# Performance work log

Hardware: AMD Instinct MI355X
Metric: run time of the kernel (lower is better)

## Reference

```python
import jax, jax.numpy as jnp
import numpy as np

HID, E, S, L_CAP, EPS = 768, 1536, 128, 512, 1e-5


def _rope_seq(x):
    """RoPE along axis 1. x: [b, n, 2, s]."""
    n, s = x.shape[1], x.shape[-1]
    half = s // 2
    inv_freq = jnp.power(10000.0, -jnp.arange(half, dtype=x.dtype) / half)  # [half]
    sinusoid = jnp.arange(n, dtype=x.dtype)[:, None, None] * inv_freq       # [n,1,half]
    sin, cos = jnp.sin(sinusoid), jnp.cos(sinusoid)
    x1, x2 = jnp.split(x, 2, axis=-1)
    return jnp.concatenate([x1 * cos - x2 * sin, x2 * cos + x1 * sin], axis=-1)


def setup_inputs() -> dict:
    key = jax.random.key(0)
    ks = jax.random.split(key, 6)
    B, L = 32, 512
    return {
        "x": jax.random.normal(ks[0], (B, L, HID), dtype=jnp.float32),
        "ln_gamma": jnp.ones((HID,), jnp.float32),
        "ln_beta": jnp.zeros((HID,), jnp.float32),
        "uv_W": jax.random.normal(ks[1], (HID, 2 * E + S), jnp.float32) * 0.02,
        "uv_b": jnp.zeros((2 * E + S,), jnp.float32),
        "gamma_qk": jax.random.normal(ks[2], (2, S), jnp.float32) * 0.02,
        "beta_qk": jnp.zeros((2, S), jnp.float32),
        "w_rel": jax.random.normal(ks[3], (2 * L_CAP - 1,), jnp.float32) * 0.02,
        "o_W": jax.random.normal(ks[4], (E, HID), jnp.float32) * 0.02,
        "o_b": jnp.zeros((HID,), jnp.float32),
    }


def reference(x, ln_gamma, ln_beta, uv_W, uv_b, gamma_qk, beta_qk, w_rel, o_W, o_b):
    L = x.shape[1]
    shortcut = x
    # LayerNorm
    mu = jnp.mean(x, axis=-1, keepdims=True)
    var = jnp.mean(jnp.square(x - mu), axis=-1, keepdims=True)
    xn = (x - mu) * jax.lax.rsqrt(var + EPS) * ln_gamma + ln_beta
    # uv projection + silu, split into u, v, base
    uv = jax.nn.silu(xn @ uv_W + uv_b)                       # [b, n, 2e+s]
    u, v, base = jnp.split(uv, [E, 2 * E], axis=-1)          # [b,n,e], [b,n,e], [b,n,s]
    # per-head affine then RoPE -> q, k
    base = base[..., None, :] * gamma_qk + beta_qk           # [b, n, 2, s]
    base = _rope_seq(base)
    q, k = base[..., 0, :], base[..., 1, :]
    # relu^2 attention kernel with Toeplitz relative position bias
    qk = jnp.einsum('bnd,bmd->bnm', q, k)
    idx = jnp.arange(L)
    bias = w_rel[idx[None, :] - idx[:, None] + L - 1]        # bias[i,j] = w[j-i+L-1]
    kernel = jnp.square(jax.nn.relu(qk / L + bias))
    # gated value aggregation + output projection + residual
    out = u * jnp.einsum('bnm,bme->bne', kernel, v)
    out = out @ o_W + o_b
    return out + shortcut
```

## Files before the change

kernel.cpp:

```cpp
#include <hip/hip_runtime.h>
#include <hip/hip_bf16.h>
#include <math.h>

typedef __bf16 bf16x8 __attribute__((ext_vector_type(8)));
typedef float f32x4 __attribute__((ext_vector_type(4)));
typedef unsigned short u16x4 __attribute__((ext_vector_type(4)));

#define AS1P const __attribute__((address_space(1))) void*
#define AS3P __attribute__((address_space(3))) void*

__device__ __forceinline__ float b2f(unsigned short h) {
    unsigned int u = ((unsigned int)h) << 16;
    return __builtin_bit_cast(float, u);
}
__device__ __forceinline__ unsigned short f2b(float f) {
    unsigned int u = __builtin_bit_cast(unsigned int, f);
    u += 0x7FFFu + ((u >> 16) & 1u);
    return (unsigned short)(u >> 16);
}
__device__ __forceinline__ float silu(float c) {
    return c * __builtin_amdgcn_rcpf(1.0f + __expf(-c));
}

__global__ __launch_bounds__(256) void k_convT(const float* __restrict__ src,
                                               unsigned short* __restrict__ dst,
                                               int R, int C) {
    __shared__ float tile[32][33];
    int tx = threadIdx.x, ty = threadIdx.y;
    int r0 = blockIdx.y << 5, c0 = blockIdx.x << 5;
#pragma unroll
    for (int i = 0; i < 4; ++i)
        tile[ty + 8 * i][tx] = src[(long long)(r0 + ty + 8 * i) * C + c0 + tx];
    __syncthreads();
#pragma unroll
    for (int i = 0; i < 4; ++i)
        dst[(long long)(c0 + ty + 8 * i) * R + r0 + tx] = f2b(tile[tx][ty + 8 * i]);
}

__global__ __launch_bounds__(256) void k_ln(const float* __restrict__ x,
                                            const float* __restrict__ g,
                                            const float* __restrict__ b,
                                            unsigned short* __restrict__ xn) {
    int row = blockIdx.x;
    int t = threadIdx.x;
    const float* xr = x + (long long)row * 768;
    float v0 = xr[t], v1 = xr[t + 256], v2 = xr[t + 512];
    float s = v0 + v1 + v2;
    float q = v0 * v0 + v1 * v1 + v2 * v2;
#pragma unroll
    for (int off = 32; off > 0; off >>= 1) {
        s += __shfl_xor(s, off);
        q += __shfl_xor(q, off);
    }
    __shared__ float ss[4], sq[4];
    int w = t >> 6;
    if ((t & 63) == 0) { ss[w] = s; sq[w] = q; }
    __syncthreads();
    float S_ = ss[0] + ss[1] + ss[2] + ss[3];
    float Q_ = sq[0] + sq[1] + sq[2] + sq[3];
    float mu = S_ * (1.0f / 768.0f);
    float var = Q_ * (1.0f / 768.0f) - mu * mu;
    float rs = rsqrtf(var + 1e-5f);
    unsigned short* xo = xn + (long long)row * 768;
    xo[t]       = f2b((v0 - mu) * rs * g[t]       + b[t]);
    xo[t + 256] = f2b((v1 - mu) * rs * g[t + 256] + b[t + 256]);
    xo[t + 512] = f2b((v2 - mu) * rs * g[t + 512] + b[t + 512]);
}

__global__ __launch_bounds__(128) void k_rope(const unsigned short* __restrict__ bS,
                                              const float* __restrict__ gqk,
                                              const float* __restrict__ bqk,
                                              unsigned short* __restrict__ q,
                                              unsigned short* __restrict__ k) {
    int row = blockIdx.x;
    int l = row & 511;
    int s = threadIdx.x;
    int j = s & 63;
    int partner = s ^ 64;
    float b0 = b2f(bS[(long long)row * 128 + s]);
    float bp = b2f(bS[(long long)row * 128 + partner]);
    float invf = __expf((float)j * -0.14391156831f);
    float th = (float)l * invf;
    float sn, cs;
    __sincosf(th, &sn, &cs);
    float sign = (s < 64) ? -1.0f : 1.0f;
    float preq  = b0 * gqk[s]           + bqk[s];
    float preqp = bp * gqk[partner]     + bqk[partner];
    q[(long long)row * 128 + s] = f2b(preq * cs + sign * preqp * sn);
    float prek  = b0 * gqk[128 + s]       + bqk[128 + s];
    float prekp = bp * gqk[128 + partner] + bqk[128 + partner];
    k[(long long)row * 128 + s] = f2b(prek * cs + sign * prekp * sn);
}

__global__ __launch_bounds__(256) void k_qk(const unsigned short* __restrict__ A,
                                            const unsigned short* __restrict__ B,
                                            const float* __restrict__ wrel,
                                            unsigned short* __restrict__ P) {
    __shared__ __align__(16) unsigned short As[128 * 64];
    __shared__ __align__(16) unsigned short Bs[128 * 64];
    int t = threadIdx.x;
    int w = t >> 6, lane = t & 63;
    int wr = w >> 1, wc = w & 1;
    int bx = blockIdx.x, by = blockIdx.y, bz = blockIdx.z;
    const unsigned short* Ab = A + (long long)bz * 512 * 128 + (long long)by * 128 * 128;
    const unsigned short* Bb = B + (long long)bz * 512 * 128 + (long long)bx * 128 * 128;

    f32x4 acc[4][4];
#pragma unroll
    for (int m = 0; m < 4; ++m)
#pragma unroll
        for (int n = 0; n < 4; ++n) acc[m][n] = (f32x4){0.f, 0.f, 0.f, 0.f};

    int rowA = (w << 3) + (lane >> 3);
    int colA = (lane & 7) << 3;

    for (int k0 = 0; k0 < 128; k0 += 64) {
#pragma unroll
        for (int i = 0; i < 4; ++i) {
            int r = (i << 5) + rowA;
            __builtin_amdgcn_global_load_lds(
                (AS1P)(Ab + (long long)r * 128 + k0 + colA),
                (AS3P)(&As[(i << 11) + (w << 9)]), 16, 0, 0);
            __builtin_amdgcn_global_load_lds(
                (AS1P)(Bb + (long long)r * 128 + k0 + colA),
                (AS3P)(&Bs[(i << 11) + (w << 9)]), 16, 0, 0);
        }
        __syncthreads();
#pragma unroll
        for (int ks = 0; ks < 2; ++ks) {
            bf16x8 af[4], bfr[4];
#pragma unroll
            for (int m = 0; m < 4; ++m)
                af[m] = *(const bf16x8*)&As[((wr << 6) + (m << 4) + (lane & 15)) * 64 +
                                            (ks << 5) + ((lane >> 4) << 3)];
#pragma unroll
            for (int n = 0; n < 4; ++n)
                bfr[n] = *(const bf16x8*)&Bs[((wc << 6) + (n << 4) + (lane & 15)) * 64 +
                                             (ks << 5) + ((lane >> 4) << 3)];
#pragma unroll
            for (int m = 0; m < 4; ++m)
#pragma unroll
                for (int n = 0; n < 4; ++n)
                    acc[m][n] = __builtin_amdgcn_mfma_f32_16x16x32_bf16(bfr[n], af[m],
                                                                        acc[m][n], 0, 0, 0);
        }
        __syncthreads();
    }

    int c15 = lane & 15, qq = lane >> 4;
    int rowb = (by << 7) + (wr << 6) + c15;
    int colb = (bx << 7) + (wc << 6) + (qq << 2);
#pragma unroll
    for (int m = 0; m < 4; ++m) {
#pragma unroll
        for (int n = 0; n < 4; ++n) {
            int grow = rowb + (m << 4);
            int gcol = colb + (n << 4);
            f32x4 a = acc[m][n];
            int base = gcol - grow + 511;
            u16x4 o;
#pragma unroll
            for (int i = 0; i < 4; ++i) {
                float val = a[i] * (1.0f / 512.0f) + wrel[base + i];
                val = fmaxf(val, 0.0f);
                o[i] = f2b(val * val);
            }
            *(u16x4*)(P + ((long long)(bz * 512 + grow)) * 512 + gcol) = o;
        }
    }
}

__device__ __forceinline__ bf16x8 ldsb(const char* p) {
    bf16x8 r;
    unsigned int off =
        (unsigned int)(unsigned long long)(__attribute__((address_space(3))) const void*)p;
    asm volatile("ds_read_b128 %0, %1" : "=v"(r) : "v"(off));
    return r;
}
__device__ __forceinline__ void stage64(const unsigned short* __restrict__ g, int ldk,
                                        char* lds, int r0, int w, int lane) {
    int row = r0 + (w << 3) + (lane >> 3);
    int colb = (lane & 7) << 4;
    int scolb = colb ^ ((row & 7) << 4);
    __builtin_amdgcn_global_load_lds(
        (AS1P)((const char*)g + (long long)row * (ldk * 2) + scolb),
        (AS3P)(lds + (r0 << 7) + (w << 10)), 16, 0, 0);
}

template <bool SWAP, int NT>
__device__ __forceinline__ void kloopP(const unsigned short* __restrict__ Ab,
                                       const unsigned short* __restrict__ Bb,
                                       char* A0, char* A1, char* B0, char* B1,
                                       f32x4 (&acc)[8][4], int tid, int wr, int wc,
                                       int o0, int o1) {
    constexpr int K = NT * 64;
    int w = tid >> 6, lane = tid & 63;
    const int abase = wr * 16384;
    const int bbase = wc * 8192;
    bf16x8 afA[2], afB[2], bfrA[4], bfrB[4];

#define STAGE(gA, gB, bufA, bufB)                          \
    stage64(gA, K, bufA, 0, w, lane);                      \
    stage64(gA, K, bufA, 64, w, lane);                     \
    stage64(gA, K, bufA, 128, w, lane);                    \
    stage64(gA, K, bufA, 192, w, lane);                    \
    stage64(gB, K, bufB, 0, w, lane);                      \
    stage64(gB, K, bufB, 64, w, lane);                     \
    stage64(gB, K, bufB, 128, w, lane);                    \
    stage64(gB, K, bufB, 192, w, lane);
#define LA(DST, mp, OKS, BUF)                              \
    DST[0] = ldsb((BUF) + abase + (mp) * 4096 + (OKS));    \
    DST[1] = ldsb((BUF) + abase + (mp) * 4096 + 2048 + (OKS));
#define LB(DST, OKS, BUF)                                  \
    DST[0] = ldsb((BUF) + bbase + (OKS));                  \
    DST[1] = ldsb((BUF) + bbase + 2048 + (OKS));           \
    DST[2] = ldsb((BUF) + bbase + 4096 + (OKS));           \
    DST[3] = ldsb((BUF) + bbase + 6144 + (OKS));
#define WAITL(N)                                           \
    asm volatile("s_waitcnt lgkmcnt(" #N ")" ::: "memory");\
    __builtin_amdgcn_sched_barrier(0);
#define MM(mp, BFR, AF)                                                               \
    __builtin_amdgcn_s_setprio(1);                                                    \
    _Pragma("unroll") for (int j_ = 0; j_ < 2; ++j_)                                  \
        _Pragma("unroll") for (int n_ = 0; n_ < 4; ++n_) {                            \
            if constexpr (SWAP)                                                       \
                acc[(mp) * 2 + j_][n_] = __builtin_amdgcn_mfma_f32_16x16x32_bf16(     \
                    BFR[n_], AF[j_], acc[(mp) * 2 + j_][n_], 0, 0, 0);                \
            else                                                                      \
                acc[(mp) * 2 + j_][n_] = __builtin_amdgcn_mfma_f32_16x16x32_bf16(     \
                    AF[j_], BFR[n_], acc[(mp) * 2 + j_][n_], 0, 0, 0);                \
        }                                                                             \
    __builtin_amdgcn_s_setprio(0);
#define TILE(CA, CB, NA, NB, t)                                                       \
    LA(afB, 1, o0, CA) WAITL(2) MM(0, bfrA, afA)                                      \
    LA(afA, 2, o0, CA) WAITL(2) MM(1, bfrA, afB)                                      \
    LA(afB, 3, o0, CA) LB(bfrB, o1, CB) WAITL(6) MM(2, bfrA, afA)                     \
    LA(afA, 0, o1, CA) WAITL(6) MM(3, bfrA, afB)                                      \
    LA(afB, 1, o1, CA) WAITL(2) MM(0, bfrB, afA)                                      \
    LA(afA, 2, o1, CA) WAITL(2) MM(1, bfrB, afB)                                      \
    LA(afB, 3, o1, CA) WAITL(2) MM(2, bfrB, afA)                                      \
    WAITL(0) MM(3, bfrB, afB)                                                         \
    __builtin_amdgcn_s_barrier();                                                     \
    if ((t) + 2 < NT) {                                                               \
        STAGE(Ab + ((t) + 2) * 64, Bb + ((t) + 2) * 64, CA, CB)                       \
        asm volatile("s_waitcnt vmcnt(8)" ::: "memory");                              \
    } else if ((t) + 1 < NT) {                                                        \
        asm volatile("s_waitcnt vmcnt(0)" ::: "memory");                              \
    }                                                                                 \
    __builtin_amdgcn_sched_barrier(0);                                                \
    if ((t) + 1 < NT) { LB(bfrA, o0, NB) LA(afA, 0, o0, NA) }

    STAGE(Ab, Bb, A0, B0)
    STAGE(Ab + 64, Bb + 64, A1, B1)
    asm volatile("s_waitcnt vmcnt(8)" ::: "memory");
    __builtin_amdgcn_s_barrier();
    LB(bfrA, o0, B0) LA(afA, 0, o0, A0)

#pragma unroll 1
    for (int t = 0; t < NT; t += 2) {
        TILE(A0, B0, A1, B1, t)
        TILE(A1, B1, A0, B0, t + 1)
    }
#undef STAGE
#undef LA
#undef LB
#undef WAITL
#undef MM
#undef TILE
}

template <int EPI, bool SWZ, int NT>
__global__ __launch_bounds__(512, 2) void kP(const unsigned short* __restrict__ A,
                                             const unsigned short* __restrict__ B,
                                             long long strideA, long long strideB,
                                             void* p0, void* p1, void* p2,
                                             const void* p3) {
    constexpr int K = NT * 64;
    __shared__ __align__(16) char As[2][256 * 128];
    __shared__ __align__(16) char Bs[2][256 * 128];
    int tid = threadIdx.x;
    int w = tid >> 6, lane = tid & 63;
    int wr = w >> 2, wc = w & 3;
    int c15 = lane & 15, qq = lane >> 4;
    int g = (c15 & 7) << 4;
    int o0 = c15 * 128 + ((qq * 16) ^ g);
    int o1 = c15 * 128 + ((64 + qq * 16) ^ g);
    int bx = blockIdx.x, by = blockIdx.y, bz = blockIdx.z;
    if constexpr (SWZ) {
        int gx = gridDim.x;
        int nb = gx * gridDim.y;
        int bid = by * gx + bx;
        int s = (bid & 7) * (nb >> 3) + (bid >> 3);
        bx = s % gx;
        by = s / gx;
    }
    const unsigned short* Ab = A + bz * strideA + (long long)by * 256 * K;
    const unsigned short* Bb = B + bz * strideB + (long long)bx * 256 * K;

    f32x4 acc[8][4];
#pragma unroll
    for (int m = 0; m < 8; ++m)
#pragma unroll
        for (int n = 0; n < 4; ++n) acc[m][n] = (f32x4){0.f, 0.f, 0.f, 0.f};

    bool swapped = true;
    if constexpr (EPI == 10) {
        swapped = !(bx >= 6 && bx < 12);
        if (swapped)
            kloopP<true, NT>(Ab, Bb, As[0], As[1], Bs[0], Bs[1], acc, tid, wr, wc, o0, o1);
        else
            kloopP<false, NT>(Ab, Bb, As[0], As[1], Bs[0], Bs[1], acc, tid, wr, wc, o0, o1);
    } else {
        kloopP<true, NT>(Ab, Bb, As[0], As[1], Bs[0], Bs[1], acc, tid, wr, wc, o0, o1);
    }

    if constexpr (EPI == 10) {
        if (swapped) {
            int rowb = by * 256 + wr * 128 + c15;
            int colb = bx * 256 + wc * 64 + (qq << 2);
#pragma unroll
            for (int m = 0; m < 8; ++m) {
#pragma unroll
                for (int n = 0; n < 4; ++n) {
                    int R = rowb + m * 16;
                    int C = colb + n * 16;
                    f32x4 a = acc[m][n];
                    if (C < 1536) {
                        f32x4 bb = *(const f32x4*)((const float*)p3 + C);
                        u16x4 o;
#pragma unroll
                        for (int i = 0; i < 4; ++i) o[i] = f2b(silu(a[i] + bb[i]));
                        *(u16x4*)((unsigned short*)p0 + (long long)R * 1536 + C) = o;
                    } else if (C < 3200) {
                        f32x4 bb = *(const f32x4*)((const float*)p3 + C);
                        u16x4 o;
#pragma unroll
                        for (int i = 0; i < 4; ++i) o[i] = f2b(silu(a[i] + bb[i]));
                        *(u16x4*)((unsigned short*)p2 + (long long)R * 128 + (C - 3072)) = o;
                    }
                }
            }
        } else {
            int rowb = by * 256 + wr * 128 + (qq << 2);
            int colb = bx * 256 + wc * 64 + c15;
#pragma unroll
            for (int m = 0; m < 8; ++m) {
#pragma unroll
                for (int n = 0; n < 4; ++n) {
                    int R = rowb + m * 16;
                    int C = colb + n * 16;
                    float bias = ((const float*)p3)[C];
                    f32x4 a = acc[m][n];
                    u16x4 o;
#pragma unroll
                    for (int i = 0; i < 4; ++i) o[i] = f2b(silu(a[i] + bias));
                    int bb2 = R >> 9, mm = R & 511;
                    *(u16x4*)((unsigned short*)p1 +
                              ((long long)bb2 * 1536 + (C - 1536)) * 512 + mm) = o;
                }
            }
        }
    } else if constexpr (EPI == 2) {
        int rowb = by * 256 + wr * 128 + c15;
        int colb = bx * 256 + wc * 64 + (qq << 2);
#pragma unroll
        for (int m = 0; m < 8; ++m) {
#pragma unroll
            for (int n = 0; n < 4; ++n) {
                int R = rowb + m * 16;
                int C = colb + n * 16;
                f32x4 a = acc[m][n];
                long long idx = ((long long)(bz * 512 + R)) * 1536 + C;
                u16x4 uu = *(const u16x4*)((const unsigned short*)p1 + idx);
                u16x4 o;
#pragma unroll
                for (int i = 0; i < 4; ++i) o[i] = f2b(a[i] * b2f(uu[i]));
                *(u16x4*)((unsigned short*)p0 + idx) = o;
            }
        }
    } else {
        int rowb = by * 256 + wr * 128 + c15;
        int colb = bx * 256 + wc * 64 + (qq << 2);
#pragma unroll
        for (int m = 0; m < 8; ++m) {
#pragma unroll
            for (int n = 0; n < 4; ++n) {
                int R = rowb + m * 16;
                int C = colb + n * 16;
                f32x4 a = acc[m][n];
                long long idx = (long long)R * 768 + C;
                f32x4 xv = *(const f32x4*)((const float*)p2 + idx);
                f32x4 ob = *(const f32x4*)((const float*)p1 + C);
                f32x4 o;
#pragma unroll
                for (int i = 0; i < 4; ++i) o[i] = a[i] + ob[i] + xv[i];
                *(f32x4*)((float*)p0 + idx) = o;
            }
        }
    }
}

extern "C" void kernel_launch(void* const* d_in, const int* in_sizes, int n_in,
                              void* d_out, int out_size, void* d_ws, size_t ws_size,
                              hipStream_t stream) {
    const float* x     = (const float*)d_in[0];
    const float* ln_g  = (const float*)d_in[1];
    const float* ln_b  = (const float*)d_in[2];
    const float* uv_W  = (const float*)d_in[3];
    const float* uv_b  = (const float*)d_in[4];
    const float* g_qk  = (const float*)d_in[5];
    const float* b_qk  = (const float*)d_in[6];
    const float* w_rel = (const float*)d_in[7];
    const float* o_W   = (const float*)d_in[8];
    const float* o_b   = (const float*)d_in[9];
    float* out = (float*)d_out;

    char* ws = (char*)d_ws;
    size_t off = 0;
    auto alloc = [&](size_t bytes) {
        void* p = ws + off;
        off += (bytes + 255) & ~(size_t)255;
        return p;
    };
    unsigned short* uvWT = (unsigned short*)alloc(3328ll * 768 * 2);
    unsigned short* oWT  = (unsigned short*)alloc(768ll * 1536 * 2);
    unsigned short* xn   = (unsigned short*)alloc(16384ll * 768 * 2);
    unsigned short* u    = (unsigned short*)alloc(16384ll * 1536 * 2);
    unsigned short* vT   = (unsigned short*)alloc(32ll * 1536 * 512 * 2);
    unsigned short* bS   = (unsigned short*)alloc(16384ll * 128 * 2);
    unsigned short* q    = (unsigned short*)alloc(32ll * 512 * 128 * 2);
    unsigned short* k    = (unsigned short*)alloc(32ll * 512 * 128 * 2);
    unsigned short* P     = xn;
    unsigned short* gated = u;

    k_convT<<<dim3(100, 24), dim3(32, 8), 0, stream>>>(uv_W, uvWT, 768, 3200);
    k_convT<<<dim3(24, 48), dim3(32, 8), 0, stream>>>(o_W, oWT, 1536, 768);
    k_ln<<<16384, 256, 0, stream>>>(x, ln_g, ln_b, xn);
    kP<10, true, 12><<<dim3(13, 64), 512, 0, stream>>>(
        xn, uvWT, 0, 0, (void*)u, (void*)vT, (void*)bS, (const void*)uv_b);
    k_rope<<<16384, 128, 0, stream>>>(bS, g_qk, b_qk, q, k);
    k_qk<<<dim3(4, 4, 32), 256, 0, stream>>>(q, k, w_rel, P);
    kP<2, false, 8><<<dim3(6, 2, 32), 512, 0, stream>>>(
        P, vT, 512ll * 512, 1536ll * 512, (void*)gated, (void*)u, nullptr, nullptr);
    kP<3, true, 24><<<dim3(3, 64), 512, 0, stream>>>(
        gated, oWT, 0, 0, (void*)out, (void*)o_b, (void*)x, nullptr);
}
```

Baseline: 293.8 us.

## Switch uv and output projection GEMMs to FP8 MFMA with scaled operands

```diff
diff --git a/kernel.cpp b/kernel.cpp
--- a/kernel.cpp
+++ b/kernel.cpp
@@ -1,10 +1,12 @@
 #include <hip/hip_runtime.h>
 #include <hip/hip_bf16.h>
+#include <hip/hip_fp8.h>
 #include <math.h>
 
 typedef __bf16 bf16x8 __attribute__((ext_vector_type(8)));
 typedef float f32x4 __attribute__((ext_vector_type(4)));
 typedef unsigned short u16x4 __attribute__((ext_vector_type(4)));
+typedef unsigned char u8;
 
 #define AS1P const __attribute__((address_space(1))) void*
 #define AS3P __attribute__((address_space(3))) void*
@@ -18,13 +20,17 @@
     u += 0x7FFFu + ((u >> 16) & 1u);
     return (unsigned short)(u >> 16);
 }
+__device__ __forceinline__ u8 f2e(float x) {
+    __hip_fp8_e4m3 h(x);
+    return (u8)h.__x;
+}
 __device__ __forceinline__ float silu(float c) {
     return c * __builtin_amdgcn_rcpf(1.0f + __expf(-c));
 }
 
-__global__ __launch_bounds__(256) void k_convT(const float* __restrict__ src,
-                                               unsigned short* __restrict__ dst,
-                                               int R, int C) {
+__global__ __launch_bounds__(256) void k_convT8(const float* __restrict__ src,
+                                                u8* __restrict__ dst,
+                                                int R, int C, float scale) {
     __shared__ float tile[32][33];
     int tx = threadIdx.x, ty = threadIdx.y;
     int r0 = blockIdx.y << 5, c0 = blockIdx.x << 5;
@@ -34,13 +40,13 @@
     __syncthreads();
 #pragma unroll
     for (int i = 0; i < 4; ++i)
-        dst[(long long)(c0 + ty + 8 * i) * R + r0 + tx] = f2b(tile[tx][ty + 8 * i]);
+        dst[(long long)(c0 + ty + 8 * i) * R + r0 + tx] = f2e(tile[tx][ty + 8 * i] * scale);
 }
 
 __global__ __launch_bounds__(256) void k_ln(const float* __restrict__ x,
                                             const float* __restrict__ g,
                                             const float* __restrict__ b,
-                                            unsigned short* __restrict__ xn) {
+                                            u8* __restrict__ xn) {
     int row = blockIdx.x;
     int t = threadIdx.x;
     const float* xr = x + (long long)row * 768;
@@ -61,10 +67,10 @@
     float mu = S_ * (1.0f / 768.0f);
     float var = Q_ * (1.0f / 768.0f) - mu * mu;
     float rs = rsqrtf(var + 1e-5f);
-    unsigned short* xo = xn + (long long)row * 768;
-    xo[t]       = f2b((v0 - mu) * rs * g[t]       + b[t]);
-    xo[t + 256] = f2b((v1 - mu) * rs * g[t + 256] + b[t + 256]);
-    xo[t + 512] = f2b((v2 - mu) * rs * g[t + 512] + b[t + 512]);
+    u8* xo = xn + (long long)row * 768;
+    xo[t]       = f2e((v0 - mu) * rs * g[t]       + b[t]);
+    xo[t + 256] = f2e((v1 - mu) * rs * g[t + 256] + b[t + 256]);
+    xo[t + 512] = f2e((v2 - mu) * rs * g[t + 512] + b[t + 512]);
 }
 
 __global__ __launch_bounds__(128) void k_rope(const unsigned short* __restrict__ bS,
@@ -187,16 +193,38 @@
         (AS3P)(lds + (r0 << 7) + (w << 10)), 16, 0, 0);
 }
 
-template <bool SWAP, int NT>
-__device__ __forceinline__ void kloopP(const unsigned short* __restrict__ Ab,
-                                       const unsigned short* __restrict__ Bb,
-                                       char* A0, char* A1, char* B0, char* B1,
-                                       f32x4 (&acc)[8][4], int tid, int wr, int wc,
-                                       int o0, int o1) {
+template <int NT>
+__global__ __launch_bounds__(512, 2) void k_pv(const unsigned short* __restrict__ A,
+                                               const unsigned short* __restrict__ B,
+                                               long long strideA, long long strideB,
+                                               u8* __restrict__ gated8,
+                                               const unsigned short* __restrict__ u) {
     constexpr int K = NT * 64;
+    __shared__ __align__(16) char As[2][256 * 128];
+    __shared__ __align__(16) char Bs[2][256 * 128];
+    int tid = threadIdx.x;
     int w = tid >> 6, lane = tid & 63;
+    int wr = w >> 2, wc = w & 3;
+    int c15 = lane & 15, qq = lane >> 4;
+    int g = (c15 & 7) << 4;
+    int o0 = c15 * 128 + ((qq * 16) ^ g);
+    int o1 = c15 * 128 + ((64 + qq * 16) ^ g);
+    int bx = blockIdx.x, by = blockIdx.y, bz = blockIdx.z;
+    const unsigned short* Ab = A + bz * strideA + (long long)by * 256 * K;
+    const unsigned short* Bb = B + bz * strideB + (long long)bx * 256 * K;
+
+    f32x4 acc[8][4];
+#pragma unroll
+    for (int m = 0; m < 8; ++m)
+#pragma unroll
+        for (int n = 0; n < 4; ++n) acc[m][n] = (f32x4){0.f, 0.f, 0.f, 0.f};
+
     const int abase = wr * 16384;
     const int bbase = wc * 8192;
+    char* A0 = As[0];
+    char* A1 = As[1];
+    char* B0 = Bs[0];
+    char* B1 = Bs[1];
     bf16x8 afA[2], afB[2], bfrA[4], bfrB[4];
 
 #define STAGE(gA, gB, bufA, bufB)                          \
@@ -222,14 +250,9 @@
 #define MM(mp, BFR, AF)                                                               \
     __builtin_amdgcn_s_setprio(1);                                                    \
     _Pragma("unroll") for (int j_ = 0; j_ < 2; ++j_)                                  \
-        _Pragma("unroll") for (int n_ = 0; n_ < 4; ++n_) {                            \
-            if constexpr (SWAP)                                                       \
-                acc[(mp) * 2 + j_][n_] = __builtin_amdgcn_mfma_f32_16x16x32_bf16(     \
-                    BFR[n_], AF[j_], acc[(mp) * 2 + j_][n_], 0, 0, 0);                \
-            else                                                                      \
-                acc[(mp) * 2 + j_][n_] = __builtin_amdgcn_mfma_f32_16x16x32_bf16(     \
-                    AF[j_], BFR[n_], acc[(mp) * 2 + j_][n_], 0, 0, 0);                \
-        }                                                                             \
+        _Pragma("unroll") for (int n_ = 0; n_ < 4; ++n_)                              \
+            acc[(mp) * 2 + j_][n_] = __builtin_amdgcn_mfma_f32_16x16x32_bf16(         \
+                BFR[n_], AF[j_], acc[(mp) * 2 + j_][n_], 0, 0, 0);                    \
     __builtin_amdgcn_s_setprio(0);
 #define TILE(CA, CB, NA, NB, t)                                                       \
     LA(afB, 1, o0, CA) WAITL(2) MM(0, bfrA, afA)                                      \
@@ -267,25 +290,65 @@
 #undef WAITL
 #undef MM
 #undef TILE
+
+    int rowb = by * 256 + wr * 128 + c15;
+    int colb = bx * 256 + wc * 64 + (qq << 2);
+#pragma unroll
+    for (int m = 0; m < 8; ++m) {
+#pragma unroll
+        for (int n = 0; n < 4; ++n) {
+            int R = rowb + m * 16;
+            int C = colb + n * 16;
+            f32x4 a = acc[m][n];
+            long long idx = ((long long)(bz * 512 + R)) * 1536 + C;
+            u16x4 uu = *(const u16x4*)(u + idx);
+            unsigned int pk = 0;
+#pragma unroll
+            for (int i = 0; i < 4; ++i)
+                pk |= ((unsigned int)f2e(a[i] * b2f(uu[i]) * 8.0f)) << (8 * i);
+            *(unsigned int*)(gated8 + idx) = pk;
+        }
+    }
+}
+
+__device__ __forceinline__ long ldsb64(const char* p) {
+    long r;
+    unsigned int off =
+        (unsigned int)(unsigned long long)(__attribute__((address_space(3))) const void*)p;
+    asm volatile("ds_read_b64 %0, %1" : "=v"(r) : "v"(off));
+    return r;
+}
+__device__ __forceinline__ const char* fraddr(const char* T, int row, int ks, int qq) {
+    int offs = ks * 32 + qq * 8;
+    int gg = offs >> 4, wb = offs & 8;
+    return T + row * 128 + (((gg ^ (row & 7)) << 4) | wb);
+}
+template <int K>
+__device__ __forceinline__ void stageF(const u8* __restrict__ g, char* lds, int tid) {
+#pragma unroll
+    for (int i = 0; i < 4; ++i) {
+        int ch = i * 512 + tid;
+        int row = ch >> 3;
+        int gg = ch & 7;
+        __builtin_amdgcn_global_load_lds(
+            (AS1P)(g + (long long)row * K + ((gg ^ (row & 7)) << 4)),
+            (AS3P)(lds + ch * 16), 16, 0, 0);
+    }
 }
 
 template <int EPI, bool SWZ, int NT>
-__global__ __launch_bounds__(512, 2) void kP(const unsigned short* __restrict__ A,
-                                             const unsigned short* __restrict__ B,
-                                             long long strideA, long long strideB,
-                                             void* p0, void* p1, void* p2,
-                                             const void* p3) {
-    constexpr int K = NT * 64;
+__global__ __launch_bounds__(512) void kF(const u8* __restrict__ A,
+                                          const u8* __restrict__ B,
+                                          void* p0, void* p1, void* p2,
+                                          const void* p3) {
+    constexpr int K = NT * 128;
     __shared__ __align__(16) char As[2][256 * 128];
     __shared__ __align__(16) char Bs[2][256 * 128];
     int tid = threadIdx.x;
     int w = tid >> 6, lane = tid & 63;
     int wr = w >> 2, wc = w & 3;
     int c15 = lane & 15, qq = lane >> 4;
-    int g = (c15 & 7) << 4;
-    int o0 = c15 * 128 + ((qq * 16) ^ g);
-    int o1 = c15 * 128 + ((64 + qq * 16) ^ g);
-    int bx = blockIdx.x, by = blockIdx.y, bz = blockIdx.z;
+    int bx = blockIdx.x, by = blockIdx.y;
     if constexpr (SWZ) {
         int gx = gridDim.x;
         int nb = gx * gridDim.y;
@@ -294,8 +357,8 @@
         bx = s % gx;
         by = s / gx;
     }
-    const unsigned short* Ab = A + bz * strideA + (long long)by * 256 * K;
-    const unsigned short* Bb = B + bz * strideB + (long long)bx * 256 * K;
+    const u8* Ab = A + (long long)by * 256 * K;
+    const u8* Bb = B + (long long)bx * 256 * K;
 
     f32x4 acc[8][4];
 #pragma unroll
@@ -303,16 +366,66 @@
 #pragma unroll
         for (int n = 0; n < 4; ++n) acc[m][n] = (f32x4){0.f, 0.f, 0.f, 0.f};
 
-    bool swapped = true;
-    if constexpr (EPI == 10) {
-        swapped = !(bx >= 6 && bx < 12);
-        if (swapped)
-            kloopP<true, NT>(Ab, Bb, As[0], As[1], Bs[0], Bs[1], acc, tid, wr, wc, o0, o1);
+    const bool swapped = (EPI != 10) || !(bx >= 6 && bx < 12);
+
+#define RDF(AF, BF, ks)                                                      \
+    _Pragma("unroll") for (int n_ = 0; n_ < 4; ++n_)                         \
+        BF[n_] = ldsb64(fraddr(Bt, wc * 64 + n_ * 16 + c15, ks, qq));        \
+    _Pragma("unroll") for (int m_ = 0; m_ < 8; ++m_)                         \
+        AF[m_] = ldsb64(fraddr(At, wr * 128 + m_ * 16 + c15, ks, qq));
+#define WAITLF(N)                                                            \
+    asm volatile("s_waitcnt lgkmcnt(" #N ")" ::: "memory");                  \
+    __builtin_amdgcn_sched_barrier(0);
+#define MMF(AF, BF)                                                          \
+    __builtin_amdgcn_s_setprio(1);                                           \
+    _Pragma("unroll") for (int m_ = 0; m_ < 8; ++m_)                         \
+        _Pragma("unroll") for (int n_ = 0; n_ < 4; ++n_) {                   \
+            if (swapped)                                                     \
+                acc[m_][n_] = __builtin_amdgcn_mfma_f32_16x16x32_fp8_fp8(    \
+                    BF[n_], AF[m_], acc[m_][n_], 0, 0, 0);                   \
+            else                                                             \
+                acc[m_][n_] = __builtin_amdgcn_mfma_f32_16x16x32_fp8_fp8(    \
+                    AF[m_], BF[n_], acc[m_][n_], 0, 0, 0);                   \
+        }                                                                    \
+    __builtin_amdgcn_s_setprio(0);
+
+    stageF<K>(Ab, As[0], tid);
+    stageF<K>(Bb, Bs[0], tid);
+    stageF<K>(Ab + 128, As[1], tid);
+    stageF<K>(Bb + 128, Bs[1], tid);
+
+#pragma unroll 1
+    for (int t = 0; t < NT; ++t) {
+        if (t < NT - 1)
+            asm volatile("s_waitcnt vmcnt(8)" ::: "memory");
         else
-            kloopP<false, NT>(Ab, Bb, As[0], As[1], Bs[0], Bs[1], acc, tid, wr, wc, o0, o1);
-    } else {
-        kloopP<true, NT>(Ab, Bb, As[0], As[1], Bs[0], Bs[1], acc, tid, wr, wc, o0, o1);
-    }
+            asm volatile("s_waitcnt vmcnt(0)" ::: "memory");
+        __builtin_amdgcn_s_barrier();
+        __builtin_amdgcn_sched_barrier(0);
+        const char* At = As[t & 1];
+        const char* Bt = Bs[t & 1];
+        long af[8], bfv[4], af2[8], bfv2[4];
+        RDF(af, bfv, 0)
+        RDF(af2, bfv2, 1)
+        WAITLF(12)
+        MMF(af, bfv)
+        RDF(af, bfv, 2)
+        WAITLF(12)
+        MMF(af2, bfv2)
+        RDF(af2, bfv2, 3)
+        WAITLF(12)
+        MMF(af, bfv)
+        WAITLF(0)
+        __builtin_amdgcn_s_barrier();
+        if (t + 2 < NT) {
+            stageF<K>(Ab + (long long)(t + 2) * 128, As[t & 1], tid);
+            stageF<K>(Bb + (long long)(t + 2) * 128, Bs[t & 1], tid);
+        }
+        MMF(af2, bfv2)
+    }
+#undef RDF
+#undef WAITLF
+#undef MMF
 
     if constexpr (EPI == 10) {
         if (swapped) {
@@ -329,13 +442,15 @@
                         f32x4 bb = *(const f32x4*)((const float*)p3 + C);
                         u16x4 o;
 #pragma unroll
-                        for (int i = 0; i < 4; ++i) o[i] = f2b(silu(a[i] + bb[i]));
+                        for (int i = 0; i < 4; ++i)
+                            o[i] = f2b(silu(a[i] * 0.03125f + bb[i]));
                         *(u16x4*)((unsigned short*)p0 + (long long)R * 1536 + C) = o;
                     } else if (C < 3200) {
                         f32x4 bb = *(const f32x4*)((const float*)p3 + C);
                         u16x4 o;
 #pragma unroll
-                        for (int i = 0; i < 4; ++i) o[i] = f2b(silu(a[i] + bb[i]));
+                        for (int i = 0; i < 4; ++i)
+                            o[i] = f2b(silu(a[i] * 0.03125f + bb[i]));
                         *(u16x4*)((unsigned short*)p2 + (long long)R * 128 + (C - 3072)) = o;
                     }
                 }
@@ -353,29 +468,12 @@
                     f32x4 a = acc[m][n];
                     u16x4 o;
 #pragma unroll
-                    for (int i = 0; i < 4; ++i) o[i] = f2b(silu(a[i] + bias));
+                    for (int i = 0; i < 4; ++i)
+                        o[i] = f2b(silu(a[i] * 0.03125f + bias));
                     int bb2 = R >> 9, mm = R & 511;
                     *(u16x4*)((unsigned short*)p1 +
                               ((long long)bb2 * 1536 + (C - 1536)) * 512 + mm) = o;
                 }
-            }
-        }
-    } else if constexpr (EPI == 2) {
-        int rowb = by * 256 + wr * 128 + c15;
-        int colb = bx * 256 + wc * 64 + (qq << 2);
-#pragma unroll
-        for (int m = 0; m < 8; ++m) {
-#pragma unroll
-            for (int n = 0; n < 4; ++n) {
-                int R = rowb + m * 16;
-                int C = colb + n * 16;
-                f32x4 a = acc[m][n];
-                long long idx = ((long long)(bz * 512 + R)) * 1536 + C;
-                u16x4 uu = *(const u16x4*)((const unsigned short*)p1 + idx);
-                u16x4 o;
-#pragma unroll
-                for (int i = 0; i < 4; ++i) o[i] = f2b(a[i] * b2f(uu[i]));
-                *(u16x4*)((unsigned short*)p0 + idx) = o;
             }
         }
     } else {
@@ -393,7 +491,7 @@
                 f32x4 ob = *(const f32x4*)((const float*)p1 + C);
                 f32x4 o;
 #pragma unroll
-                for (int i = 0; i < 4; ++i) o[i] = a[i] + ob[i] + xv[i];
+                for (int i = 0; i < 4; ++i) o[i] = a[i] * 0.00390625f + ob[i] + xv[i];
                 *(f32x4*)((float*)p0 + idx) = o;
             }
         }
@@ -422,26 +520,26 @@
         off += (bytes + 255) & ~(size_t)255;
         return p;
     };
-    unsigned short* uvWT = (unsigned short*)alloc(3328ll * 768 * 2);
-    unsigned short* oWT  = (unsigned short*)alloc(768ll * 1536 * 2);
-    unsigned short* xn   = (unsigned short*)alloc(16384ll * 768 * 2);
-    unsigned short* u    = (unsigned short*)alloc(16384ll * 1536 * 2);
-    unsigned short* vT   = (unsigned short*)alloc(32ll * 1536 * 512 * 2);
-    unsigned short* bS   = (unsigned short*)alloc(16384ll * 128 * 2);
-    unsigned short* q    = (unsigned short*)alloc(32ll * 512 * 128 * 2);
-    unsigned short* k    = (unsigned short*)alloc(32ll * 512 * 128 * 2);
-    unsigned short* P     = xn;
-    unsigned short* gated = u;
-
-    k_convT<<<dim3(100, 24), dim3(32, 8), 0, stream>>>(uv_W, uvWT, 768, 3200);
-    k_convT<<<dim3(24, 48), dim3(32, 8), 0, stream>>>(o_W, oWT, 1536, 768);
-    k_ln<<<16384, 256, 0, stream>>>(x, ln_g, ln_b, xn);
-    kP<10, true, 12><<<dim3(13, 64), 512, 0, stream>>>(
-        xn, uvWT, 0, 0, (void*)u, (void*)vT, (void*)bS, (const void*)uv_b);
+    u8* xn8    = (u8*)alloc(16384ll * 768);
+    u8* uvWT8  = (u8*)alloc(3328ll * 768);
+    unsigned short* bS = (unsigned short*)alloc(16384ll * 128 * 2);
+    u8* oWT8   = (u8*)alloc(768ll * 1536);
+    unsigned short* u  = (unsigned short*)alloc(16384ll * 1536 * 2);
+    unsigned short* vT = (unsigned short*)alloc(32ll * 1536 * 512 * 2);
+    unsigned short* q  = (unsigned short*)alloc(32ll * 512 * 128 * 2);
+    unsigned short* k  = (unsigned short*)alloc(32ll * 512 * 128 * 2);
+    u8* gated8 = (u8*)alloc(16384ll * 1536);
+    unsigned short* P = (unsigned short*)xn8;
+
+    k_convT8<<<dim3(100, 24), dim3(32, 8), 0, stream>>>(uv_W, uvWT8, 768, 3200, 32.0f);
+    k_convT8<<<dim3(24, 48), dim3(32, 8), 0, stream>>>(o_W, oWT8, 1536, 768, 32.0f);
+    k_ln<<<16384, 256, 0, stream>>>(x, ln_g, ln_b, xn8);
+    kF<10, true, 6><<<dim3(13, 64), 512, 0, stream>>>(
+        xn8, uvWT8, (void*)u, (void*)vT, (void*)bS, (const void*)uv_b);
     k_rope<<<16384, 128, 0, stream>>>(bS, g_qk, b_qk, q, k);
     k_qk<<<dim3(4, 4, 32), 256, 0, stream>>>(q, k, w_rel, P);
-    kP<2, false, 8><<<dim3(6, 2, 32), 512, 0, stream>>>(
-        P, vT, 512ll * 512, 1536ll * 512, (void*)gated, (void*)u, nullptr, nullptr);
-    kP<3, true, 24><<<dim3(3, 64), 512, 0, stream>>>(
-        gated, oWT, 0, 0, (void*)out, (void*)o_b, (void*)x, nullptr);
-}
+    k_pv<8><<<dim3(6, 2, 32), 512, 0, stream>>>(
+        P, vT, 512ll * 512, 1536ll * 512, gated8, u);
+    kF<3, true, 12><<<dim3(3, 64), 512, 0, stream>>>(
+        gated8, oWT8, (void*)out, (void*)o_b, (void*)x, nullptr);
+}
```

Result: slower. 797.2 us (+171.4%).
